# Performance work log

Hardware: AMD Instinct MI355X
Metric: run time of the kernel (lower is better)

## Reference

```python
import jax, jax.numpy as jnp
import numpy as np

N = 100000
E = 3200000
IN_C, HID_C, OUT_C = 128, 128, 64


def setup_inputs() -> dict:
    key = jax.random.key(0)
    k_x, k_e, k_w1, k_w2 = jax.random.split(key, 4)
    x = jax.random.normal(k_x, (N, IN_C), dtype=jnp.float32)
    edge_index = jax.random.randint(k_e, (2, E), 0, N, dtype=jnp.int64)
    # GCNConv uses Glorot-init weight [in, out] and zero bias
    W1 = jax.random.normal(k_w1, (IN_C, HID_C), dtype=jnp.float32) * (1.0 / np.sqrt(IN_C))
    b1 = jnp.zeros((HID_C,), dtype=jnp.float32)
    W2 = jax.random.normal(k_w2, (HID_C, OUT_C), dtype=jnp.float32) * (1.0 / np.sqrt(HID_C))
    b2 = jnp.zeros((OUT_C,), dtype=jnp.float32)
    return {"x": x, "edge_index": edge_index, "W1": W1, "b1": b1, "W2": W2, "b2": b2}


def _gcn_norm(edge_index, n_nodes):
    """Add self-loops and compute symmetric normalization coefficients."""
    loop = jnp.arange(n_nodes, dtype=edge_index.dtype)
    src = jnp.concatenate([edge_index[0], loop])  # [E+N]
    dst = jnp.concatenate([edge_index[1], loop])  # [E+N]
    ones = jnp.ones(src.shape[0], dtype=jnp.float32)
    deg = jax.ops.segment_sum(ones, dst, num_segments=n_nodes)  # in-degree w/ self loops
    dinv = jnp.where(deg > 0, jax.lax.rsqrt(deg), 0.0)
    norm = dinv[src] * dinv[dst]  # [E+N]
    return src, dst, norm


def _gcn_conv(x, W, b, src, dst, norm, n_nodes):
    h = x @ W                                   # [N, out] dense transform first (PyG order)
    msg = norm[:, None] * h[src]                # gather + scale  [E+N, out]
    out = jax.ops.segment_sum(msg, dst, num_segments=n_nodes)  # scatter-add
    return out + b


def reference(x, edge_index, W1, b1, W2, b2):
    src, dst, norm = _gcn_norm(edge_index, N)
    h = _gcn_conv(x, W1, b1, src, dst, norm, N)
    h = jax.nn.relu(h)
    out = _gcn_conv(h, W2, b2, src, dst, norm, N)
    return out
```

## Files before the change

kernel.cpp:

```cpp
#include <hip/hip_runtime.h>

typedef unsigned int u32;
typedef unsigned short u16;
typedef unsigned long long u64;
typedef __bf16 bf16x8 __attribute__((ext_vector_type(8)));
typedef float floatx4 __attribute__((ext_vector_type(4)));
typedef u32 u32x2 __attribute__((ext_vector_type(2)));
typedef float floatx2 __attribute__((ext_vector_type(2)));

__device__ __forceinline__ u16 f2bf(float f) {
  u32 u = __float_as_uint(f);
  u += 0x7fffu + ((u >> 16) & 1u);
  return (u16)(u >> 16);
}
__device__ __forceinline__ float bf2f(u16 h) { return __uint_as_float(((u32)h) << 16); }
__device__ __forceinline__ float bflo(u32 v) { return __uint_as_float(v << 16); }
__device__ __forceinline__ float bfhi(u32 v) { return __uint_as_float(v & 0xffff0000u); }

#define SLICE_SH 10
#define SL (1 << SLICE_SH)
#define MAXNS 128

__global__ void probe_dtypes(const u16* __restrict__ xs, const u32* __restrict__ eis,
                             int* __restrict__ flags, int* __restrict__ scnt,
                             int* __restrict__ scur) {
  int lane = threadIdx.x;
  if (lane < MAXNS) { scnt[lane] = 0; scur[lane] = 0; }
  if (lane >= 64) return;
  int big = 0;
  for (int i = lane; i < 4096; i += 64) {
    u32 e = (xs[i] >> 7) & 0xffu;
    big += (e >= 0xC0u) ? 1 : 0;
  }
  int odd = 0;
  for (int i = lane; i < 256; i += 64)
    odd += (eis[2 * i + 1] != 0u) ? 1 : 0;
#pragma unroll
  for (int off = 32; off; off >>= 1) {
    big += __shfl_down(big, off);
    odd += __shfl_down(odd, off);
  }
  if (lane == 0 && blockIdx.x == 0) {
    flags[0] = (big > 16) ? 1 : 0;
    flags[1] = (odd == 0) ? 1 : 0;
  }
}


__global__ __launch_bounds__(256) void hist_pass(const int* __restrict__ ei,
                                                 const int* __restrict__ flags,
                                                 int* __restrict__ scnt, int e, int ns) {
  __shared__ int hist[MAXNS];
  int per = (e + gridDim.x - 1) / gridDim.x;
  int e0 = blockIdx.x * per;
  int e1 = e0 + per; if (e1 > e) e1 = e;
  for (int t = threadIdx.x; t < ns; t += 256) hist[t] = 0;
  __syncthreads();
  const int i64f = flags[1];
  for (int i = e0 + threadIdx.x; i < e1; i += 256) {
    int d = i64f ? ei[2 * (e + i)] : ei[e + i];
    atomicAdd(&hist[d >> SLICE_SH], 1);
  }
  __syncthreads();
  for (int t = threadIdx.x; t < ns; t += 256)
    atomicAdd(&scnt[t], hist[t]);
}

__global__ __launch_bounds__(128) void scan_slices(const int* __restrict__ scnt,
                                                   int* __restrict__ sbase,
                                                   int* __restrict__ rp,
                                                   int e, int n, int ns) {
  __shared__ int sm[MAXNS];
  int t = threadIdx.x;
  sm[t] = (t < ns) ? scnt[t] : 0;
  __syncthreads();
  for (int off = 1; off < MAXNS; off <<= 1) {
    int v = (t >= off) ? sm[t - off] : 0;
    __syncthreads();
    sm[t] += v;
    __syncthreads();
  }
  if (t <= ns) sbase[t] = t ? sm[t - 1] : 0;
  if (t == 0) rp[n] = e;
}

__global__ __launch_bounds__(256) void bin_pass(const int* __restrict__ ei,
                                                const int* __restrict__ flags,
                                                const int* __restrict__ sbase,
                                                int* __restrict__ scur,
                                                u64* __restrict__ staged,
                                                int e, int ns) {
  __shared__ int hist[MAXNS];
  __shared__ int curs[MAXNS];
  int per = (e + gridDim.x - 1) / gridDim.x;
  int e0 = blockIdx.x * per;
  int e1 = e0 + per; if (e1 > e) e1 = e;
  const int i64f = flags[1];
  for (int t = threadIdx.x; t < ns; t += 256) hist[t] = 0;
  __syncthreads();
  for (int i = e0 + threadIdx.x; i < e1; i += 256) {
    int d = i64f ? ei[2 * (e + i)] : ei[e + i];
    atomicAdd(&hist[d >> SLICE_SH], 1);
  }
  __syncthreads();
  for (int t = threadIdx.x; t < ns; t += 256)
    curs[t] = sbase[t] + atomicAdd(&scur[t], hist[t]);
  __syncthreads();
  int i = e0 + threadIdx.x;
  for (; i + 768 < e1; i += 1024) {
    int d[4], s[4], pos[4];
#pragma unroll
    for (int p = 0; p < 4; p++) {
      int ii = i + 256 * p;
      if (i64f) { s[p] = ei[2 * ii]; d[p] = ei[2 * (e + ii)]; }
      else      { s[p] = ei[ii];     d[p] = ei[e + ii]; }
    }
#pragma unroll
    for (int p = 0; p < 4; p++) pos[p] = atomicAdd(&curs[d[p] >> SLICE_SH], 1);
#pragma unroll
    for (int p = 0; p < 4; p++)
      staged[pos[p]] = ((u64)(u32)d[p] << 32) | (u32)s[p];
  }
  for (; i < e1; i += 256) {
    int s, d;
    if (i64f) { s = ei[2 * i]; d = ei[2 * (e + i)]; }
    else      { s = ei[i];     d = ei[e + i]; }
    staged[atomicAdd(&curs[d >> SLICE_SH], 1)] = ((u64)(u32)d << 32) | (u32)s;
  }
}

__global__ __launch_bounds__(1024) void fill_slice2(const u64* __restrict__ staged,
                                                    const int* __restrict__ sbase,
                                                    int* __restrict__ rp,
                                                    float* __restrict__ dinv,
                                                    int* __restrict__ csr, int n, int ns) {
  __shared__ int cnt[SL];
  __shared__ int part[SL];
  const int s = blockIdx.x;
  const int base = s << SLICE_SH;
  const int lo = sbase[s], hi = sbase[s + 1];
  const int tid = threadIdx.x;
  cnt[tid] = 0;
  __syncthreads();
  {
    int i = lo + tid;
    for (; i + 7168 < hi; i += 8192) {
      int b[8];
#pragma unroll
      for (int p = 0; p < 8; p++) b[p] = (int)(staged[i + 1024 * p] >> 32) & (SL - 1);
#pragma unroll
      for (int p = 0; p < 8; p++) atomicAdd(&cnt[b[p]], 1);
    }
    for (; i < hi; i += 1024)
      atomicAdd(&cnt[(int)(staged[i] >> 32) & (SL - 1)], 1);
  }
  __syncthreads();
  int c0 = cnt[tid];
  part[tid] = c0;
  __syncthreads();
  for (int off = 1; off < SL; off <<= 1) {
    int t = (tid >= off) ? part[tid - off] : 0;
    __syncthreads();
    part[tid] += t;
    __syncthreads();
  }
  int p0 = lo + (tid ? part[tid - 1] : 0);
  __syncthreads();
  cnt[tid] = p0;
  int d0 = base + tid;
  if (d0 < n) { rp[d0] = p0; dinv[d0] = rsqrtf((float)(c0 + 1)); }
  __syncthreads();
  {
    int i = lo + tid;
    for (; i + 7168 < hi; i += 8192) {
      u64 pr[8]; int pos[8];
#pragma unroll
      for (int p = 0; p < 8; p++) pr[p] = staged[i + 1024 * p];
#pragma unroll
      for (int p = 0; p < 8; p++)
        pos[p] = atomicAdd(&cnt[(int)(pr[p] >> 32) & (SL - 1)], 1);
#pragma unroll
      for (int p = 0; p < 8; p++) csr[pos[p]] = (int)(pr[p] & 0xffffffffu);
    }
    for (; i < hi; i += 1024) {
      u64 pr = staged[i];
      int pos = atomicAdd(&cnt[(int)(pr >> 32) & (SL - 1)], 1);
      csr[pos] = (int)(pr & 0xffffffffu);
    }
  }
}


template <int OUT, bool XPROBED>
__global__ __launch_bounds__(256) void gemm_x_w(const void* __restrict__ Xv,
                                                const void* __restrict__ Wv,
                                                const int* __restrict__ flags,
                                                u16* __restrict__ Y, int nrows) {
  constexpr int K = 128;
  constexpr int NT = OUT / 16;
  constexpr int LDW = K + 8;
  __shared__ u16 Wt[OUT * LDW];
  const int wf32 = flags[0];
  const int xf32 = XPROBED ? wf32 : 0;
  int tid = threadIdx.x;
  if (wf32) {
    const float* Wf = (const float*)Wv;
    for (int idx = tid; idx < K * OUT; idx += 256) {
      int k = idx / OUT, n = idx % OUT;
      Wt[n * LDW + k] = f2bf(Wf[idx]);
    }
  } else {
    const u16* Wu = (const u16*)Wv;
    for (int idx = tid; idx < K * OUT; idx += 256) {
      int k = idx / OUT, n = idx % OUT;
      Wt[n * LDW + k] = Wu[idx];
    }
  }
  __syncthreads();
  int lane = tid & 63, wave = tid >> 6;
  int quad = lane >> 4, low = lane & 15;
  int mBase = blockIdx.x * 64 + wave * 16;
  int m = mBase + low;
  int ml = (m < nrows) ? m : (nrows - 1);
  floatx4 acc[NT];
#pragma unroll
  for (int i = 0; i < NT; i++) acc[i] = (floatx4)0.0f;
#pragma unroll
  for (int kb = 0; kb < 4; kb++) {
    int k0 = kb * 32 + quad * 8;
    bf16x8 a;
    if (xf32) {
      const float* Xf = (const float*)Xv;
      floatx4 p0 = *(const floatx4*)(Xf + (size_t)ml * K + k0);
      floatx4 p1 = *(const floatx4*)(Xf + (size_t)ml * K + k0 + 4);
      union { bf16x8 v; u16 s[8]; } au;
#pragma unroll
      for (int j = 0; j < 4; j++) { au.s[j] = f2bf(p0[j]); au.s[4 + j] = f2bf(p1[j]); }
      a = au.v;
    } else {
      a = *(const bf16x8*)((const u16*)Xv + (size_t)ml * K + k0);
    }
#pragma unroll
    for (int nt = 0; nt < NT; nt++) {
      bf16x8 b = *(const bf16x8*)(&Wt[(nt * 16 + low) * LDW + k0]);
      acc[nt] = __builtin_amdgcn_mfma_f32_16x16x32_bf16(a, b, acc[nt], 0, 0, 0);
    }
  }
#pragma unroll
  for (int nt = 0; nt < NT; nt++) {
    int col = nt * 16 + low;
#pragma unroll
    for (int r = 0; r < 4; r++) {
      int row = mBase + quad * 4 + r;
      if (row < nrows) Y[(size_t)row * OUT + col] = f2bf(acc[nt][r]);
    }
  }
}


__global__ __launch_bounds__(256) void agg_128(const u32* __restrict__ H,
                                               const int* __restrict__ rp,
                                               const int* __restrict__ cs,
                                               const float* __restrict__ dinv,
                                               const void* __restrict__ biasv,
                                               const int* __restrict__ flags,
                                               u32* __restrict__ out, int n) {
  int node = blockIdx.x * 4 + (threadIdx.x >> 6);
  if (node >= n) return;
  int lane = threadIdx.x & 63;
  int eh = lane >> 5, c = lane & 31;
  int s0 = rp[node], s1 = rp[node + 1];
  float a0 = 0.f, a1 = 0.f, a2 = 0.f, a3 = 0.f;
  for (int base = s0; base < s1; base += 64) {
    int nb = s1 - base; if (nb > 64) nb = 64;
    int src = 0; float dv = 0.f;
    if (lane < nb) { src = cs[base + lane]; dv = dinv[src]; }
    for (int j = 0; j < nb; j += 16) {
      u32x2 v[8]; float w[8];
#pragma unroll
      for (int p = 0; p < 8; p++) {
        int idx = j + 2 * p + eh;
        int sj = __shfl(src, idx);
        w[p] = __shfl(dv, idx);
        v[p] = *(const u32x2*)(H + (size_t)sj * 64 + 2 * c);
      }
#pragma unroll
      for (int p = 0; p < 8; p++) {
        a0 += w[p] * bflo(v[p].x); a1 += w[p] * bfhi(v[p].x);
        a2 += w[p] * bflo(v[p].y); a3 += w[p] * bfhi(v[p].y);
      }
    }
  }
  a0 += __shfl_xor(a0, 32); a1 += __shfl_xor(a1, 32);
  a2 += __shfl_xor(a2, 32); a3 += __shfl_xor(a3, 32);
  float ds = dinv[node];
  u32x2 vs = *(const u32x2*)(H + (size_t)node * 64 + 2 * c);
  float r0 = ds * (a0 + ds * bflo(vs.x));
  float r1 = ds * (a1 + ds * bfhi(vs.x));
  float r2 = ds * (a2 + ds * bflo(vs.y));
  float r3 = ds * (a3 + ds * bfhi(vs.y));
  float b0, b1, b2, b3;
  if (flags[0]) {
    floatx4 bf = *(const floatx4*)((const float*)biasv + 4 * c);
    b0 = bf[0]; b1 = bf[1]; b2 = bf[2]; b3 = bf[3];
  } else {
    u32x2 bb = *(const u32x2*)((const u32*)biasv + 2 * c);
    b0 = bflo(bb.x); b1 = bfhi(bb.x); b2 = bflo(bb.y); b3 = bfhi(bb.y);
  }
  r0 = fmaxf(r0 + b0, 0.f); r1 = fmaxf(r1 + b1, 0.f);
  r2 = fmaxf(r2 + b2, 0.f); r3 = fmaxf(r3 + b3, 0.f);
  if (eh == 0) {
    u32x2 o;
    o.x = (u32)f2bf(r0) | ((u32)f2bf(r1) << 16);
    o.y = (u32)f2bf(r2) | ((u32)f2bf(r3) << 16);
    *(u32x2*)(out + (size_t)node * 64 + 2 * c) = o;
  }
}

__global__ __launch_bounds__(256) void agg_64(const u16* __restrict__ Hu,
                                              const int* __restrict__ rp,
                                              const int* __restrict__ cs,
                                              const float* __restrict__ dinv,
                                              const void* __restrict__ biasv,
                                              const int* __restrict__ flags,
                                              void* __restrict__ outv, int n) {
  const u32* H = (const u32*)Hu;
  int node = blockIdx.x * 4 + (threadIdx.x >> 6);
  if (node >= n) return;
  int lane = threadIdx.x & 63;
  int eh = lane >> 5, c = lane & 31;
  int s0 = rp[node], s1 = rp[node + 1];
  float a0 = 0.f, a1 = 0.f;
  for (int base = s0; base < s1; base += 64) {
    int nb = s1 - base; if (nb > 64) nb = 64;
    int src = 0; float dv = 0.f;
    if (lane < nb) { src = cs[base + lane]; dv = dinv[src]; }
    for (int j = 0; j < nb; j += 16) {
      u32 v[8]; float w[8];
#pragma unroll
      for (int p = 0; p < 8; p++) {
        int idx = j + 2 * p + eh;
        int sj = __shfl(src, idx);
        w[p] = __shfl(dv, idx);
        v[p] = H[(size_t)sj * 32 + c];
      }
#pragma unroll
      for (int p = 0; p < 8; p++) {
        a0 += w[p] * bflo(v[p]); a1 += w[p] * bfhi(v[p]);
      }
    }
  }
  a0 += __shfl_xor(a0, 32); a1 += __shfl_xor(a1, 32);
  float ds = dinv[node];
  u32 vs = H[(size_t)node * 32 + c];
  float r0 = ds * (a0 + ds * bflo(vs));
  float r1 = ds * (a1 + ds * bfhi(vs));
  if (flags[0]) {
    floatx2 bf = *(const floatx2*)((const float*)biasv + 2 * c);
    r0 += bf[0]; r1 += bf[1];
    if (eh == 0) {
      floatx2 o; o[0] = r0; o[1] = r1;
      *(floatx2*)((float*)outv + (size_t)node * 64 + 2 * c) = o;
    }
  } else {
    u32 bb = ((const u32*)biasv)[c];
    r0 += bflo(bb); r1 += bfhi(bb);
    if (eh == 0)
      ((u32*)outv)[(size_t)node * 32 + c] = (u32)f2bf(r0) | ((u32)f2bf(r1) << 16);
  }
}


extern "C" void kernel_launch(void* const* d_in, const int* in_sizes, int n_in,
                              void* d_out, int out_size, void* d_ws, size_t ws_size,
                              hipStream_t stream) {
  const void* x  = d_in[0];
  const int*  ei = (const int*)d_in[1];
  const void* W1 = d_in[2];
  const void* b1 = d_in[3];
  const void* W2 = d_in[4];
  const void* b2 = d_in[5];
  const int N = in_sizes[0] / 128;
  const int E = in_sizes[1] / 2;
  const int NS = (N + SL - 1) >> SLICE_SH;

  auto al = [](size_t v) { return (v + 255) & ~(size_t)255; };
  char* ws = (char*)d_ws;
  size_t o = 0;
  int*   flags = (int*)(ws + o);  o += 256;
  int*   scnt  = (int*)(ws + o);  o += 512;
  int*   sbase = (int*)(ws + o);  o += 768;
  int*   scur  = (int*)(ws + o);  o += 512;
  int*   rp    = (int*)(ws + o);  o += al((size_t)(N + 1) * 4);
  float* dinv  = (float*)(ws + o); o += al((size_t)N * 4);
  int*   csr   = (int*)(ws + o);  o += al((size_t)E * 4);
  u16*   h     = (u16*)(ws + o);  o += al((size_t)N * 128 * 2);
  u16*   h1    = (u16*)(ws + o);  o += al((size_t)N * 128 * 2);
  u16*   h2    = h;
  u64* staged = (u64*)h;

  probe_dtypes<<<1, 128, 0, stream>>>((const u16*)x, (const u32*)ei, flags, scnt, scur);
  hist_pass<<<1280, 256, 0, stream>>>(ei, flags, scnt, E, NS);
  scan_slices<<<1, 128, 0, stream>>>(scnt, sbase, rp, E, N, NS);
  bin_pass<<<1280, 256, 0, stream>>>(ei, flags, sbase, scur, staged, E, NS);
  fill_slice2<<<NS, 1024, 0, stream>>>(staged, sbase, rp, dinv, csr, N, NS);

  gemm_x_w<128, true><<<(N + 63) / 64, 256, 0, stream>>>(x, W1, flags, h, N);
  agg_128<<<(N + 3) / 4, 256, 0, stream>>>((const u32*)h, rp, csr, dinv, b1, flags, (u32*)h1, N);
  gemm_x_w<64, false><<<(N + 63) / 64, 256, 0, stream>>>(h1, W2, flags, h2, N);
  agg_64<<<(N + 3) / 4, 256, 0, stream>>>(h2, rp, csr, dinv, b2, flags, d_out, N);
}
```

Before: 424.5 us.

## Fold slice scan into consumers and widen aggregation gathers to 16-byte loads

Removes the single-block scan_slices launch. bin_pass and fill_slice2 now each redo the small 128-entry prefix scan in shared memory, and fill_slice2 writes rp[n] itself. The aggregation kernels now process four edges in parallel per wavefront, with 16 lanes per row issuing 16-byte (agg_128) or 8-byte (agg_64) loads instead of 8/4-byte ones. A second xor-shuffle stage reduces the partial sums. This trades one launch plus fewer, wider gather transactions for redundant per-block scan work and more reduction shuffles.

```diff
diff --git a/kernel.cpp b/kernel.cpp
--- a/kernel.cpp
+++ b/kernel.cpp
@@ -6,6 +6,7 @@
 typedef __bf16 bf16x8 __attribute__((ext_vector_type(8)));
 typedef float floatx4 __attribute__((ext_vector_type(4)));
 typedef u32 u32x2 __attribute__((ext_vector_type(2)));
+typedef u32 u32x4 __attribute__((ext_vector_type(4)));
 typedef float floatx2 __attribute__((ext_vector_type(2)));
 
 __device__ __forceinline__ u16 f2bf(float f) {
@@ -66,45 +67,36 @@
     atomicAdd(&scnt[t], hist[t]);
 }
 
-__global__ __launch_bounds__(128) void scan_slices(const int* __restrict__ scnt,
-                                                   int* __restrict__ sbase,
-                                                   int* __restrict__ rp,
-                                                   int e, int n, int ns) {
-  __shared__ int sm[MAXNS];
-  int t = threadIdx.x;
-  sm[t] = (t < ns) ? scnt[t] : 0;
-  __syncthreads();
-  for (int off = 1; off < MAXNS; off <<= 1) {
-    int v = (t >= off) ? sm[t - off] : 0;
-    __syncthreads();
-    sm[t] += v;
-    __syncthreads();
-  }
-  if (t <= ns) sbase[t] = t ? sm[t - 1] : 0;
-  if (t == 0) rp[n] = e;
-}
-
 __global__ __launch_bounds__(256) void bin_pass(const int* __restrict__ ei,
                                                 const int* __restrict__ flags,
-                                                const int* __restrict__ sbase,
+                                                const int* __restrict__ scnt,
                                                 int* __restrict__ scur,
                                                 u64* __restrict__ staged,
                                                 int e, int ns) {
   __shared__ int hist[MAXNS];
   __shared__ int curs[MAXNS];
+  __shared__ int sb[MAXNS];
   int per = (e + gridDim.x - 1) / gridDim.x;
   int e0 = blockIdx.x * per;
   int e1 = e0 + per; if (e1 > e) e1 = e;
   const int i64f = flags[1];
   for (int t = threadIdx.x; t < ns; t += 256) hist[t] = 0;
+  if (threadIdx.x < MAXNS) sb[threadIdx.x] = (threadIdx.x < ns) ? scnt[threadIdx.x] : 0;
   __syncthreads();
   for (int i = e0 + threadIdx.x; i < e1; i += 256) {
     int d = i64f ? ei[2 * (e + i)] : ei[e + i];
     atomicAdd(&hist[d >> SLICE_SH], 1);
   }
   __syncthreads();
+  for (int off = 1; off < MAXNS; off <<= 1) {
+    int v = 0;
+    if (threadIdx.x < MAXNS && threadIdx.x >= off) v = sb[threadIdx.x - off];
+    __syncthreads();
+    if (threadIdx.x < MAXNS) sb[threadIdx.x] += v;
+    __syncthreads();
+  }
   for (int t = threadIdx.x; t < ns; t += 256)
-    curs[t] = sbase[t] + atomicAdd(&scur[t], hist[t]);
+    curs[t] = (t ? sb[t - 1] : 0) + atomicAdd(&scur[t], hist[t]);
   __syncthreads();
   int i = e0 + threadIdx.x;
   for (; i + 768 < e1; i += 1024) {
@@ -130,18 +122,29 @@
 }
 
 __global__ __launch_bounds__(1024) void fill_slice2(const u64* __restrict__ staged,
-                                                    const int* __restrict__ sbase,
+                                                    const int* __restrict__ scnt,
                                                     int* __restrict__ rp,
                                                     float* __restrict__ dinv,
                                                     int* __restrict__ csr, int n, int ns) {
   __shared__ int cnt[SL];
   __shared__ int part[SL];
+  __shared__ int sb[MAXNS];
   const int s = blockIdx.x;
   const int base = s << SLICE_SH;
-  const int lo = sbase[s], hi = sbase[s + 1];
   const int tid = threadIdx.x;
   cnt[tid] = 0;
-  __syncthreads();
+  if (tid < MAXNS) sb[tid] = (tid < ns) ? scnt[tid] : 0;
+  __syncthreads();
+  for (int off = 1; off < MAXNS; off <<= 1) {
+    int v = 0;
+    if (tid < MAXNS && tid >= off) v = sb[tid - off];
+    __syncthreads();
+    if (tid < MAXNS) sb[tid] += v;
+    __syncthreads();
+  }
+  const int lo = s ? sb[s - 1] : 0;
+  const int hi = sb[s];
+  if (s == ns - 1 && tid == 0) rp[n] = hi;
   {
     int i = lo + tid;
     for (; i + 7168 < hi; i += 8192) {
@@ -268,52 +271,63 @@
   int node = blockIdx.x * 4 + (threadIdx.x >> 6);
   if (node >= n) return;
   int lane = threadIdx.x & 63;
-  int eh = lane >> 5, c = lane & 31;
+  int e4 = lane >> 4, c = lane & 15;
   int s0 = rp[node], s1 = rp[node + 1];
-  float a0 = 0.f, a1 = 0.f, a2 = 0.f, a3 = 0.f;
+  float a[8] = {0.f, 0.f, 0.f, 0.f, 0.f, 0.f, 0.f, 0.f};
   for (int base = s0; base < s1; base += 64) {
     int nb = s1 - base; if (nb > 64) nb = 64;
     int src = 0; float dv = 0.f;
     if (lane < nb) { src = cs[base + lane]; dv = dinv[src]; }
     for (int j = 0; j < nb; j += 16) {
-      u32x2 v[8]; float w[8];
-#pragma unroll
-      for (int p = 0; p < 8; p++) {
-        int idx = j + 2 * p + eh;
+      u32x4 v[4]; float w[4];
+#pragma unroll
+      for (int p = 0; p < 4; p++) {
+        int idx = j + 4 * p + e4;
         int sj = __shfl(src, idx);
         w[p] = __shfl(dv, idx);
-        v[p] = *(const u32x2*)(H + (size_t)sj * 64 + 2 * c);
+        v[p] = *(const u32x4*)(H + (size_t)sj * 64 + 4 * c);
       }
 #pragma unroll
-      for (int p = 0; p < 8; p++) {
-        a0 += w[p] * bflo(v[p].x); a1 += w[p] * bfhi(v[p].x);
-        a2 += w[p] * bflo(v[p].y); a3 += w[p] * bfhi(v[p].y);
+      for (int p = 0; p < 4; p++) {
+#pragma unroll
+        for (int k = 0; k < 4; k++) {
+          a[2 * k]     += w[p] * bflo(v[p][k]);
+          a[2 * k + 1] += w[p] * bfhi(v[p][k]);
+        }
       }
     }
   }
-  a0 += __shfl_xor(a0, 32); a1 += __shfl_xor(a1, 32);
-  a2 += __shfl_xor(a2, 32); a3 += __shfl_xor(a3, 32);
+#pragma unroll
+  for (int k = 0; k < 8; k++) {
+    a[k] += __shfl_xor(a[k], 16);
+    a[k] += __shfl_xor(a[k], 32);
+  }
   float ds = dinv[node];
-  u32x2 vs = *(const u32x2*)(H + (size_t)node * 64 + 2 * c);
-  float r0 = ds * (a0 + ds * bflo(vs.x));
-  float r1 = ds * (a1 + ds * bfhi(vs.x));
-  float r2 = ds * (a2 + ds * bflo(vs.y));
-  float r3 = ds * (a3 + ds * bfhi(vs.y));
-  float b0, b1, b2, b3;
+  u32x4 vs = *(const u32x4*)(H + (size_t)node * 64 + 4 * c);
+  float r[8];
+#pragma unroll
+  for (int k = 0; k < 4; k++) {
+    r[2 * k]     = ds * (a[2 * k]     + ds * bflo(vs[k]));
+    r[2 * k + 1] = ds * (a[2 * k + 1] + ds * bfhi(vs[k]));
+  }
   if (flags[0]) {
-    floatx4 bf = *(const floatx4*)((const float*)biasv + 4 * c);
-    b0 = bf[0]; b1 = bf[1]; b2 = bf[2]; b3 = bf[3];
+    floatx4 b0 = *(const floatx4*)((const float*)biasv + 8 * c);
+    floatx4 b1 = *(const floatx4*)((const float*)biasv + 8 * c + 4);
+#pragma unroll
+    for (int k = 0; k < 4; k++) { r[k] += b0[k]; r[4 + k] += b1[k]; }
   } else {
-    u32x2 bb = *(const u32x2*)((const u32*)biasv + 2 * c);
-    b0 = bflo(bb.x); b1 = bfhi(bb.x); b2 = bflo(bb.y); b3 = bfhi(bb.y);
-  }
-  r0 = fmaxf(r0 + b0, 0.f); r1 = fmaxf(r1 + b1, 0.f);
-  r2 = fmaxf(r2 + b2, 0.f); r3 = fmaxf(r3 + b3, 0.f);
-  if (eh == 0) {
-    u32x2 o;
-    o.x = (u32)f2bf(r0) | ((u32)f2bf(r1) << 16);
-    o.y = (u32)f2bf(r2) | ((u32)f2bf(r3) << 16);
-    *(u32x2*)(out + (size_t)node * 64 + 2 * c) = o;
+    u32x4 bb = *(const u32x4*)((const u32*)biasv + 4 * c);
+#pragma unroll
+    for (int k = 0; k < 4; k++) { r[2 * k] += bflo(bb[k]); r[2 * k + 1] += bfhi(bb[k]); }
+  }
+#pragma unroll
+  for (int k = 0; k < 8; k++) r[k] = fmaxf(r[k], 0.f);
+  if (e4 == 0) {
+    u32x4 o;
+#pragma unroll
+    for (int k = 0; k < 4; k++)
+      o[k] = (u32)f2bf(r[2 * k]) | ((u32)f2bf(r[2 * k + 1]) << 16);
+    *(u32x4*)(out + (size_t)node * 64 + 4 * c) = o;
   }
 }
 
@@ -328,45 +342,56 @@
   int node = blockIdx.x * 4 + (threadIdx.x >> 6);
   if (node >= n) return;
   int lane = threadIdx.x & 63;
-  int eh = lane >> 5, c = lane & 31;
+  int e4 = lane >> 4, c = lane & 15;
   int s0 = rp[node], s1 = rp[node + 1];
-  float a0 = 0.f, a1 = 0.f;
+  float a[4] = {0.f, 0.f, 0.f, 0.f};
   for (int base = s0; base < s1; base += 64) {
     int nb = s1 - base; if (nb > 64) nb = 64;
     int src = 0; float dv = 0.f;
     if (lane < nb) { src = cs[base + lane]; dv = dinv[src]; }
     for (int j = 0; j < nb; j += 16) {
-      u32 v[8]; float w[8];
-#pragma unroll
-      for (int p = 0; p < 8; p++) {
-        int idx = j + 2 * p + eh;
+      u32x2 v[4]; float w[4];
+#pragma unroll
+      for (int p = 0; p < 4; p++) {
+        int idx = j + 4 * p + e4;
         int sj = __shfl(src, idx);
         w[p] = __shfl(dv, idx);
-        v[p] = H[(size_t)sj * 32 + c];
+        v[p] = *(const u32x2*)(H + (size_t)sj * 32 + 2 * c);
       }
 #pragma unroll
-      for (int p = 0; p < 8; p++) {
-        a0 += w[p] * bflo(v[p]); a1 += w[p] * bfhi(v[p]);
+      for (int p = 0; p < 4; p++) {
+        a[0] += w[p] * bflo(v[p].x); a[1] += w[p] * bfhi(v[p].x);
+        a[2] += w[p] * bflo(v[p].y); a[3] += w[p] * bfhi(v[p].y);
       }
     }
   }
-  a0 += __shfl_xor(a0, 32); a1 += __shfl_xor(a1, 32);
+#pragma unroll
+  for (int k = 0; k < 4; k++) {
+    a[k] += __shfl_xor(a[k], 16);
+    a[k] += __shfl_xor(a[k], 32);
+  }
   float ds = dinv[node];
-  u32 vs = H[(size_t)node * 32 + c];
-  float r0 = ds * (a0 + ds * bflo(vs));
-  float r1 = ds * (a1 + ds * bfhi(vs));
+  u32x2 vs = *(const u32x2*)(H + (size_t)node * 32 + 2 * c);
+  float r0 = ds * (a[0] + ds * bflo(vs.x));
+  float r1 = ds * (a[1] + ds * bfhi(vs.x));
+  float r2 = ds * (a[2] + ds * bflo(vs.y));
+  float r3 = ds * (a[3] + ds * bfhi(vs.y));
   if (flags[0]) {
-    floatx2 bf = *(const floatx2*)((const float*)biasv + 2 * c);
-    r0 += bf[0]; r1 += bf[1];
-    if (eh == 0) {
-      floatx2 o; o[0] = r0; o[1] = r1;
-      *(floatx2*)((float*)outv + (size_t)node * 64 + 2 * c) = o;
+    floatx4 bf = *(const floatx4*)((const float*)biasv + 4 * c);
+    r0 += bf[0]; r1 += bf[1]; r2 += bf[2]; r3 += bf[3];
+    if (e4 == 0) {
+      floatx4 o; o[0] = r0; o[1] = r1; o[2] = r2; o[3] = r3;
+      *(floatx4*)((float*)outv + (size_t)node * 64 + 4 * c) = o;
     }
   } else {
-    u32 bb = ((const u32*)biasv)[c];
-    r0 += bflo(bb); r1 += bfhi(bb);
-    if (eh == 0)
-      ((u32*)outv)[(size_t)node * 32 + c] = (u32)f2bf(r0) | ((u32)f2bf(r1) << 16);
+    u32x2 bb = *(const u32x2*)((const u32*)biasv + 2 * c);
+    r0 += bflo(bb.x); r1 += bfhi(bb.x); r2 += bflo(bb.y); r3 += bfhi(bb.y);
+    if (e4 == 0) {
+      u32x2 o;
+      o.x = (u32)f2bf(r0) | ((u32)f2bf(r1) << 16);
+      o.y = (u32)f2bf(r2) | ((u32)f2bf(r3) << 16);
+      *(u32x2*)((u32*)outv + (size_t)node * 32 + 2 * c) = o;
+    }
   }
 }
 
@@ -389,7 +414,6 @@
   size_t o = 0;
   int*   flags = (int*)(ws + o);  o += 256;
   int*   scnt  = (int*)(ws + o);  o += 512;
-  int*   sbase = (int*)(ws + o);  o += 768;
   int*   scur  = (int*)(ws + o);  o += 512;
   int*   rp    = (int*)(ws + o);  o += al((size_t)(N + 1) * 4);
   float* dinv  = (float*)(ws + o); o += al((size_t)N * 4);
@@ -401,9 +425,8 @@
 
   probe_dtypes<<<1, 128, 0, stream>>>((const u16*)x, (const u32*)ei, flags, scnt, scur);
   hist_pass<<<1280, 256, 0, stream>>>(ei, flags, scnt, E, NS);
-  scan_slices<<<1, 128, 0, stream>>>(scnt, sbase, rp, E, N, NS);
-  bin_pass<<<1280, 256, 0, stream>>>(ei, flags, sbase, scur, staged, E, NS);
-  fill_slice2<<<NS, 1024, 0, stream>>>(staged, sbase, rp, dinv, csr, N, NS);
+  bin_pass<<<1280, 256, 0, stream>>>(ei, flags, scnt, scur, staged, E, NS);
+  fill_slice2<<<NS, 1024, 0, stream>>>(staged, scnt, rp, dinv, csr, N, NS);
 
   gemm_x_w<128, true><<<(N + 63) / 64, 256, 0, stream>>>(x, W1, flags, h, N);
   agg_128<<<(N + 3) / 4, 256, 0, stream>>>((const u32*)h, rp, csr, dinv, b1, flags, (u32*)h1, N);
```

Measured after the change: 425.3 us. No clear change (+0.2%).
